# Kernel tuning notes

Hardware: AMD Instinct MI355X
Metric: run time of the kernel (lower is better)

The kernel has to match this reference:

```python
import jax, jax.numpy as jnp
import numpy as np

N_WIN = 7    # n_win hardcoded in AR_Attention
TOPK = 4     # topk routing windows
HEADS = 8    # num_heads


def setup_inputs() -> dict:
    key = jax.random.key(0)
    ks = jax.random.split(key, 6)
    B, H, W, C = 4, 56, 56, 256
    s = 0.02
    x = jax.random.normal(ks[0], (B, H, W, C), jnp.float32)
    Wqkv = jax.random.normal(ks[1], (C, 3 * C), jnp.float32) * s  # Linear(dim, 3*dim) (qk_dim=dim)
    bqkv = jnp.zeros((3 * C,), jnp.float32)
    Wo = jax.random.normal(ks[2], (C, C), jnp.float32) * s        # output projection Linear(dim, dim)
    bo = jnp.zeros((C,), jnp.float32)
    lepe_w = jax.random.normal(ks[3], (5, 5, 1, C), jnp.float32) * s  # 5x5 depthwise conv (side_dwconv=5)
    lepe_b = jnp.zeros((C,), jnp.float32)
    return {"x": x, "Wqkv": Wqkv, "bqkv": bqkv, "Wo": Wo, "bo": bo,
            "lepe_w": lepe_w, "lepe_b": lepe_b}


def reference(x, Wqkv, bqkv, Wo, bo, lepe_w, lepe_b):
    B, H, W, C = x.shape
    nw = N_WIN
    h, w = H // nw, W // nw           # region size (8x8)
    p2 = nw * nw                      # number of regions (49)
    hd = C // HEADS                   # head dim
    scale = float(C) ** -0.5          # qk_scale = qk_dim ** -0.5 (qk_dim = dim)

    # region partition: [B,H,W,C] -> [B,p2,h,w,C]
    xr = x.reshape(B, nw, h, nw, w, C).transpose(0, 1, 3, 2, 4, 5).reshape(B, p2, h, w, C)

    qkv = xr @ Wqkv + bqkv            # [B,p2,h,w,3C]
    q, kv = qkv[..., :C], qkv[..., C:]

    q_pix = q.reshape(B, p2, h * w, C)
    kv_pix = kv.reshape(B, p2, h * w, 2 * C)   # kv_downsample_mode='identity'

    # region-level queries/keys via per-window mean pooling
    q_win = q.mean((2, 3))                     # [B,p2,C]
    k_win = kv[..., :C].mean((2, 3))           # [B,p2,C]

    # LEPE: 5x5 depthwise conv on v over the full image grid
    v_img = kv[..., C:].reshape(B, nw, nw, h, w, C).transpose(0, 1, 3, 2, 4, 5).reshape(B, H, W, C)
    lepe = jax.lax.conv_general_dilated(
        v_img, lepe_w, (1, 1), 'SAME',
        dimension_numbers=('NHWC', 'HWIO', 'NHWC'),
        feature_group_count=C) + lepe_b

    # top-k window routing (param_routing=False, hard routing, mul_weight='none')
    r_logit = jnp.einsum('bpc,bqc->bpq', q_win * scale, k_win)  # [B,p2,p2]
    _, r_idx = jax.lax.top_k(r_logit, TOPK)                     # [B,p2,TOPK]

    # gather selected kv windows: [B,p2,TOPK,h*w,2C]
    kv_sel = jax.vmap(lambda kvp, i: kvp[i])(kv_pix, r_idx)

    k_sel = kv_sel[..., :C].reshape(B, p2, TOPK * h * w, HEADS, hd)
    v_sel = kv_sel[..., C:].reshape(B, p2, TOPK * h * w, HEADS, hd)
    qh = q_pix.reshape(B, p2, h * w, HEADS, hd)

    attn = jnp.einsum('bpqnd,bpknd->bpnqk', qh * scale, k_sel)  # [B,p2,heads,hw,TOPK*hw]
    attn = jax.nn.softmax(attn, axis=-1)
    out = jnp.einsum('bpnqk,bpknd->bpqnd', attn, v_sel).reshape(B, p2, h, w, C)

    # windows back to image grid
    out = out.reshape(B, nw, nw, h, w, C).transpose(0, 1, 3, 2, 4, 5).reshape(B, H, W, C)
    out = out + lepe
    return out @ Wo + bo
```

## Files before the change

kernel.cpp:

```cpp
#include <hip/hip_runtime.h>
#include <hip/hip_bf16.h>

#define NPIX 12544

typedef short bf16x8 __attribute__((ext_vector_type(8)));
typedef short bf16x4 __attribute__((ext_vector_type(4)));
typedef float f32x4  __attribute__((ext_vector_type(4)));

__device__ __forceinline__ float bf2f(unsigned short u) {
    unsigned int x = ((unsigned int)u) << 16;
    float f; __builtin_memcpy(&f, &x, sizeof(f)); return f;
}
__device__ __forceinline__ unsigned short f2bf(float f) {
    __hip_bfloat16 h = __float2bfloat16(f);
    unsigned short u; __builtin_memcpy(&u, &h, 2); return u;
}
__device__ __forceinline__ void load_lds16(const unsigned short* g, unsigned short* l) {
    __builtin_amdgcn_global_load_lds(
        (const __attribute__((address_space(1))) unsigned int*)g,
        (__attribute__((address_space(3))) unsigned int*)l,
        16, 0, 0);
}
__device__ __forceinline__ unsigned ldsoff(const void* p) {
    return (unsigned)(unsigned long long)(const __attribute__((address_space(3))) char*)p;
}
template<int OFF>
__device__ __forceinline__ bf16x4 tr16(unsigned addr) {
    bf16x4 d;
    asm volatile("ds_read_b64_tr_b16 %0, %1 offset:%c2"
                 : "=v"(d) : "v"(addr), "i"(OFF));
    return d;
}

__global__ __launch_bounds__(256) void k_prep(
    const float* __restrict__ X, unsigned short* __restrict__ Xb,
    float* __restrict__ xmean,
    const float* __restrict__ Wqkv, const float* __restrict__ Wo,
    unsigned short* __restrict__ Wtq, unsigned short* __restrict__ Wto)
{
    __shared__ __align__(16) unsigned char sm[64 * 65 * 4];
    const int t = threadIdx.x;
    const int blk = blockIdx.x;
    if (blk < 392) {
        float* part = (float*)sm;
        const int w = blk >> 1, hc = blk & 1;
        const int b = w / 49, p = w % 49;
        const int wi = p / 7, wj = p % 7;
        const int ch0 = hc * 128;
        const int ps = t >> 5, cg = t & 31;
        float4 s = {0.f, 0.f, 0.f, 0.f};
        #pragma unroll
        for (int i = 0; i < 8; i++) {
            int pp = ps * 8 + i;
            int y = wi * 8 + (pp >> 3), x = wj * 8 + (pp & 7);
            int idx = (((b * 56) + y) * 56 + x) * 256 + ch0 + cg * 4;
            float4 v = *reinterpret_cast<const float4*>(X + idx);
            s.x += v.x; s.y += v.y; s.z += v.z; s.w += v.w;
            ushort4 o = { f2bf(v.x), f2bf(v.y), f2bf(v.z), f2bf(v.w) };
            *reinterpret_cast<ushort4*>(Xb + idx) = o;
        }
        *reinterpret_cast<float4*>(part + t * 4) = *reinterpret_cast<float4*>(&s);
        __syncthreads();
        if (t < 32) {
            float4 m = {0.f, 0.f, 0.f, 0.f};
            #pragma unroll
            for (int ps2 = 0; ps2 < 8; ps2++) {
                float4 v = *reinterpret_cast<float4*>(part + (ps2 * 32 + t) * 4);
                m.x += v.x; m.y += v.y; m.z += v.z; m.w += v.w;
            }
            m.x *= (1.f / 64.f); m.y *= (1.f / 64.f);
            m.z *= (1.f / 64.f); m.w *= (1.f / 64.f);
            *reinterpret_cast<float4*>(xmean + w * 256 + ch0 + t * 4) = m;
        }
    } else {
        float* tile = (float*)sm;
        int tb = blk - 392;
        const float* Wsrc; unsigned short* Wdst; int N, kt, nt;
        if (tb < 48) { Wsrc = Wqkv; Wdst = Wtq; N = 768; kt = tb / 12; nt = tb % 12; }
        else { tb -= 48; Wsrc = Wo; Wdst = Wto; N = 256; kt = tb / 4; nt = tb % 4; }
        const int k0 = kt * 64, n0 = nt * 64;
        const int r0 = t >> 6, c = t & 63;
        #pragma unroll
        for (int i = 0; i < 16; i++) {
            int r = i * 4 + r0;
            tile[r * 65 + c] = Wsrc[(size_t)(k0 + r) * N + n0 + c];
        }
        __syncthreads();
        #pragma unroll
        for (int i = 0; i < 16; i++) {
            int n = i * 4 + r0;
            Wdst[(size_t)(n0 + n) * 256 + k0 + c] = f2bf(tile[c * 65 + n]);
        }
    }
}

__global__ __launch_bounds__(256) void k_main1(
    const unsigned short* __restrict__ A,
    const unsigned short* __restrict__ Bt,
    const float* __restrict__ bias,
    unsigned short* __restrict__ O,
    const float* __restrict__ xmean,
    const float* __restrict__ Wqkv,
    float* __restrict__ qwin, float* __restrict__ kwin)
{
    __shared__ __align__(16) unsigned char sm1[32768];
    const int t = threadIdx.x;
    const int blk = blockIdx.x;
    if (blk < 588) {
        unsigned short* As = (unsigned short*)sm1;
        unsigned short* Bs = (unsigned short*)(sm1 + 16384);
        const int m0 = (blk % 98) * 128, n0 = (blk / 98) * 128;
        const int wave = t >> 6, lane = t & 63, quad = lane >> 4, lo = lane & 15;
        const int wm = wave & 1, wn = wave >> 1;
        const int sr = wave * 16 + (lane >> 2);
        const int sc = lane & 3;
        f32x4 acc[4][4];
        #pragma unroll
        for (int i = 0; i < 4; i++)
            #pragma unroll
            for (int j = 0; j < 4; j++) acc[i][j] = (f32x4){0.f, 0.f, 0.f, 0.f};

        auto stage = [&](int it) {
            int kt = it * 32;
            unsigned short* Ad = As + (it & 1) * 4096;
            unsigned short* Bd = Bs + (it & 1) * 4096;
            #pragma unroll
            for (int j = 0; j < 2; j++) {
                int row = j * 64 + sr;
                int e = sc ^ ((row >> 1) & 3);
                load_lds16(A  + (size_t)(m0 + row) * 256 + kt + e * 8, &Ad[row * 32 + sc * 8]);
                load_lds16(Bt + (size_t)(n0 + row) * 256 + kt + e * 8, &Bd[row * 32 + sc * 8]);
            }
        };
        stage(0);
        for (int it = 0; it < 8; ++it) {
            if (it < 7) {
                stage(it + 1);
                asm volatile("s_waitcnt vmcnt(4)" ::: "memory");
            } else {
                asm volatile("s_waitcnt vmcnt(0)" ::: "memory");
            }
            __builtin_amdgcn_s_barrier();
            const unsigned short* Ac = As + (it & 1) * 4096;
            const unsigned short* Bc = Bs + (it & 1) * 4096;
            bf16x8 af[4], bfr[4];
            #pragma unroll
            for (int mt = 0; mt < 4; mt++) {
                int row = wm * 64 + mt * 16 + lo;
                int c = quad ^ ((row >> 1) & 3);
                af[mt] = *reinterpret_cast<const bf16x8*>(&Ac[row * 32 + c * 8]);
            }
            #pragma unroll
            for (int nt = 0; nt < 4; nt++) {
                int col = wn * 64 + nt * 16 + lo;
                int c = quad ^ ((col >> 1) & 3);
                bfr[nt] = *reinterpret_cast<const bf16x8*>(&Bc[col * 32 + c * 8]);
            }
            #pragma unroll
            for (int mt = 0; mt < 4; mt++)
                #pragma unroll
                for (int nt = 0; nt < 4; nt++)
                    acc[mt][nt] = __builtin_amdgcn_mfma_f32_16x16x32_bf16(
                        af[mt], bfr[nt], acc[mt][nt], 0, 0, 0);
            __builtin_amdgcn_s_barrier();
        }
        float bv[4];
        #pragma unroll
        for (int nt = 0; nt < 4; nt++) bv[nt] = bias[n0 + wn * 64 + nt * 16 + lo];
        #pragma unroll
        for (int mt = 0; mt < 4; mt++)
            #pragma unroll
            for (int nt = 0; nt < 4; nt++) {
                int n = n0 + wn * 64 + nt * 16 + lo;
                #pragma unroll
                for (int r = 0; r < 4; r++) {
                    int m = m0 + wm * 64 + mt * 16 + quad * 4 + r;
                    O[m * 768 + n] = f2bf(acc[mt][nt][r] + bv[nt]);
                }
            }
    } else {
        float* xs = (float*)sm1;
        const int u = blk - 588;
        const int bp = u % 196;
        const int half = u / 196;
        const int c = t;
        xs[c] = xmean[bp * 256 + c];
        __syncthreads();
        const int col = half * 256 + c;
        float a = 0.f;
        for (int k = 0; k < 256; k++) a += xs[k] * Wqkv[k * 768 + col];
        float* outp = half ? kwin : qwin;
        outp[bp * 256 + c] = a + bias[col];
    }
}

__global__ __launch_bounds__(256) void k_main2(
    const float* __restrict__ qwin, const float* __restrict__ kwin,
    int* __restrict__ ridx,
    const unsigned short* __restrict__ QKV,
    const float* __restrict__ lw, const float* __restrict__ lb,
    unsigned short* __restrict__ Olepe)
{
    __shared__ __align__(16) unsigned char sm2[25600];
    const int t = threadIdx.x;
    const int blk = blockIdx.x;
    if (blk < 196) {
        float* part = (float*)sm2;
        float* lg   = (float*)(sm2 + 49 * 4 * 4);
        const int b = blk / 49, p = blk % 49;
        if (t < 196) {
            int d = t >> 2, pr = t & 3;
            const float* qp = &qwin[(b * 49 + p) * 256];
            const float* kp = &kwin[(b * 49 + d) * 256];
            float a = 0.f;
            for (int ch = pr * 64; ch < pr * 64 + 64; ch++) a += qp[ch] * kp[ch];
            part[d * 4 + pr] = a;
        }
        __syncthreads();
        if (t < 49) lg[t] = part[t * 4 + 0] + part[t * 4 + 1] + part[t * 4 + 2] + part[t * 4 + 3];
        __syncthreads();
        if (t == 0) {
            unsigned long long used = 0ull;
            for (int sel = 0; sel < 4; sel++) {
                float best = -1e30f; int bi = 0;
                for (int qq = 0; qq < 49; qq++)
                    if (!((used >> qq) & 1ull) && lg[qq] > best) { best = lg[qq]; bi = qq; }
                used |= (1ull << bi);
                ridx[blk * 4 + sel] = bi;
            }
        }
    } else {
        float* lws = (float*)sm2;
        #pragma unroll
        for (int i = 0; i < 25; i++) lws[i * 256 + t] = lw[i * 256 + t];

        const int pl = t & 7;
        const int cg = t >> 3;
        const int c0 = cg * 8;
        const int gid = (blk - 196) * 8 + pl;
        const int b = gid / 3136, rem = gid % 3136;
        const int y = rem / 56, x = rem % 56;
        __syncthreads();

        float acc[8];
        {
            float4 b0 = *reinterpret_cast<const float4*>(lb + c0);
            float4 b1 = *reinterpret_cast<const float4*>(lb + c0 + 4);
            acc[0] = b0.x; acc[1] = b0.y; acc[2] = b0.z; acc[3] = b0.w;
            acc[4] = b1.x; acc[5] = b1.y; acc[6] = b1.z; acc[7] = b1.w;
        }
        #pragma unroll
        for (int ky = 0; ky < 5; ky++) {
            int yy = y + ky - 2;
            if (yy < 0 || yy >= 56) continue;
            #pragma unroll
            for (int kx = 0; kx < 5; kx++) {
                int xx = x + kx - 2;
                if (xx < 0 || xx >= 56) continue;
                bf16x8 v = *reinterpret_cast<const bf16x8*>(
                    QKV + (((b * 56) + yy) * 56 + xx) * 768 + 512 + c0);
                const float* wrow = &lws[(ky * 5 + kx) * 256 + c0];
                float4 w0 = *reinterpret_cast<const float4*>(wrow);
                float4 w1 = *reinterpret_cast<const float4*>(wrow + 4);
                acc[0] += bf2f((unsigned short)v[0]) * w0.x;
                acc[1] += bf2f((unsigned short)v[1]) * w0.y;
                acc[2] += bf2f((unsigned short)v[2]) * w0.z;
                acc[3] += bf2f((unsigned short)v[3]) * w0.w;
                acc[4] += bf2f((unsigned short)v[4]) * w1.x;
                acc[5] += bf2f((unsigned short)v[5]) * w1.y;
                acc[6] += bf2f((unsigned short)v[6]) * w1.z;
                acc[7] += bf2f((unsigned short)v[7]) * w1.w;
            }
        }
        bf16x8 o;
        #pragma unroll
        for (int j = 0; j < 8; j++) o[j] = (short)f2bf(acc[j]);
        *reinterpret_cast<bf16x8*>(Olepe + (size_t)gid * 256 + c0) = o;
    }
}

__global__ __launch_bounds__(256) void k_attn(
    const unsigned short* __restrict__ QKV,
    const int* __restrict__ ridx,
    const unsigned short* __restrict__ Olepe,
    unsigned short* __restrict__ Osum)
{
    __shared__ __align__(16) unsigned char smem[36864];
    unsigned short* Vs  = (unsigned short*)smem;
    unsigned short* Ks  = (unsigned short*)(smem + 16384);
    unsigned short* PST = (unsigned short*)(smem + 32768);

    const int p = blockIdx.x, head = blockIdx.y, b = blockIdx.z;
    const int t = threadIdx.x;
    const int wi = p / 7, wj = p % 7;
    const int wave = t >> 6, lane = t & 63, quad = lane >> 4, lo = lane & 15;
    const int pix4 = t >> 2, c4 = t & 3;

    const int q  = wave * 16 + lo;
    const int qy = wi * 8 + (q >> 3), qx = wj * 8 + (q & 7);

    bf16x8 af = *reinterpret_cast<const bf16x8*>(
        QKV + (size_t)(((b * 56) + qy) * 56 + qx) * 768 + head * 32 + quad * 8);

    {
        const int4 rs = *reinterpret_cast<const int4*>(&ridx[(b * 49 + p) * 4]);
        const int sels[4] = { rs.x, rs.y, rs.z, rs.w };
        #pragma unroll
        for (int pass = 0; pass < 4; pass++) {
            int sel = sels[pass];
            int si = sel / 7, sj = sel % 7;
            int y = si * 8 + (pix4 >> 3), x = sj * 8 + (pix4 & 7);
            const unsigned short* base = QKV + (((b * 56) + y) * 56 + x) * 768 + 256 + head * 32;
            bf16x8 kv = *reinterpret_cast<const bf16x8*>(base + c4 * 8);
            bf16x8 vv = *reinterpret_cast<const bf16x8*>(base + 256 + c4 * 8);
            int krow = pass * 64 + pix4;
            *reinterpret_cast<bf16x8*>(&Ks[krow * 32 + c4 * 8]) = kv;
            *reinterpret_cast<bf16x8*>(
                &Vs[(krow >> 2) * 128 + (c4 >> 1) * 64 + (krow & 3) * 16 + (c4 & 1) * 8]) = vv;
        }
    }
    __syncthreads();

    const f32x4 z = (f32x4){0.f, 0.f, 0.f, 0.f};

    float M[4] = {-1e30f, -1e30f, -1e30f, -1e30f};
    #pragma unroll 4
    for (int nt = 0; nt < 16; nt++) {
        bf16x8 bfr = *reinterpret_cast<const bf16x8*>(&Ks[(nt * 16 + lo) * 32 + quad * 8]);
        f32x4 s = __builtin_amdgcn_mfma_f32_16x16x32_bf16(af, bfr, z, 0, 0, 0);
        #pragma unroll
        for (int r = 0; r < 4; r++) M[r] = fmaxf(M[r], s[r] * 0.0625f);
    }
    #pragma unroll
    for (int d = 1; d < 16; d <<= 1)
        #pragma unroll
        for (int r = 0; r < 4; r++) M[r] = fmaxf(M[r], __shfl_xor(M[r], d));

    unsigned short* myP = PST + wave * 512;
    const unsigned pbase = ldsoff(myP) + quad * 256 + lo * 8;
    const unsigned vbase = ldsoff(Vs)  + quad * 512 + lo * 8;
    float l[4] = {0.f, 0.f, 0.f, 0.f};
    f32x4 o0 = z, o1 = z;
    for (int c = 0; c < 8; c++) {
        bf16x8 k0 = *reinterpret_cast<const bf16x8*>(&Ks[((2 * c) * 16 + lo) * 32 + quad * 8]);
        bf16x8 k1 = *reinterpret_cast<const bf16x8*>(&Ks[((2 * c + 1) * 16 + lo) * 32 + quad * 8]);
        f32x4 s0 = __builtin_amdgcn_mfma_f32_16x16x32_bf16(af, k0, z, 0, 0, 0);
        f32x4 s1 = __builtin_amdgcn_mfma_f32_16x16x32_bf16(af, k1, z, 0, 0, 0);
        float e0[4], e1[4];
        #pragma unroll
        for (int r = 0; r < 4; r++) {
            e0[r] = __expf(s0[r] * 0.0625f - M[r]);
            e1[r] = __expf(s1[r] * 0.0625f - M[r]);
            l[r] += e0[r] + e1[r];
        }
        ushort4 p0 = { f2bf(e0[0]), f2bf(e0[1]), f2bf(e0[2]), f2bf(e0[3]) };
        ushort4 p1 = { f2bf(e1[0]), f2bf(e1[1]), f2bf(e1[2]), f2bf(e1[3]) };
        *reinterpret_cast<ushort4*>(&myP[lo * 16 + quad * 4]) = p0;
        *reinterpret_cast<ushort4*>(&myP[(16 + lo) * 16 + quad * 4]) = p1;
        asm volatile("s_waitcnt lgkmcnt(0)" ::: "memory");
        __builtin_amdgcn_sched_barrier(0);

        const unsigned vb = vbase + c * 2048;
        bf16x4 ra0  = tr16<0>(pbase);
        bf16x4 ra1  = tr16<128>(pbase);
        bf16x4 rw00 = tr16<0>(vb);
        bf16x4 rw01 = tr16<256>(vb);
        bf16x4 rw10 = tr16<128>(vb);
        bf16x4 rw11 = tr16<384>(vb);
        asm volatile("s_waitcnt lgkmcnt(0)" ::: "memory");
        __builtin_amdgcn_sched_barrier(0);
        bf16x8 pa, vb0, vb1;
        #pragma unroll
        for (int j = 0; j < 4; j++) {
            pa[j]  = ra0[j];  pa[4 + j]  = ra1[j];
            vb0[j] = rw00[j]; vb0[4 + j] = rw01[j];
            vb1[j] = rw10[j]; vb1[4 + j] = rw11[j];
        }
        o0 = __builtin_amdgcn_mfma_f32_16x16x32_bf16(pa, vb0, o0, 0, 0, 0);
        o1 = __builtin_amdgcn_mfma_f32_16x16x32_bf16(pa, vb1, o1, 0, 0, 0);
    }
    #pragma unroll
    for (int d = 1; d < 16; d <<= 1)
        #pragma unroll
        for (int r = 0; r < 4; r++) l[r] += __shfl_xor(l[r], d);

    {
        float i0 = 1.f / l[0], i1 = 1.f / l[1], i2 = 1.f / l[2], i3 = 1.f / l[3];
        ushort4 p0 = { f2bf(o0[0] * i0), f2bf(o0[1] * i1),
                       f2bf(o0[2] * i2), f2bf(o0[3] * i3) };
        ushort4 p1 = { f2bf(o1[0] * i0), f2bf(o1[1] * i1),
                       f2bf(o1[2] * i2), f2bf(o1[3] * i3) };
        *reinterpret_cast<ushort4*>(&myP[lo * 16 + quad * 4]) = p0;
        *reinterpret_cast<ushort4*>(&myP[(16 + lo) * 16 + quad * 4]) = p1;
    }
    const unsigned oaddr = ldsoff(myP) + quad * 256 + lo * 8;
    asm volatile("s_waitcnt lgkmcnt(0)" ::: "memory");
    __builtin_amdgcn_sched_barrier(0);
    bf16x4 e0 = tr16<0>(oaddr);
    bf16x4 e1 = tr16<128>(oaddr);
    asm volatile("s_waitcnt lgkmcnt(0)" ::: "memory");
    __builtin_amdgcn_sched_barrier(0);
    {
        size_t gbase = (size_t)(((b * 56) + qy) * 56 + qx) * 256 + head * 32 + quad * 8;
        bf16x8 lp = *reinterpret_cast<const bf16x8*>(Olepe + gbase);
        bf16x8 oo;
        #pragma unroll
        for (int j = 0; j < 4; j++) {
            oo[j]     = (short)f2bf(bf2f((unsigned short)e0[j]) + bf2f((unsigned short)lp[j]));
            oo[4 + j] = (short)f2bf(bf2f((unsigned short)e1[j]) + bf2f((unsigned short)lp[4 + j]));
        }
        *reinterpret_cast<bf16x8*>(Osum + gbase) = oo;
    }
}

__global__ __launch_bounds__(256) void k_proj(
    const unsigned short* __restrict__ A,
    const unsigned short* __restrict__ Bt,
    const float* __restrict__ bias,
    float* __restrict__ O)
{
    __shared__ __align__(16) unsigned short As[2 * 128 * 32];
    __shared__ __align__(16) unsigned short Bs[2 * 64 * 32];
    const int t = threadIdx.x;
    const int m0 = blockIdx.x * 128, n0 = blockIdx.y * 64;
    const int wave = t >> 6, lane = t & 63, quad = lane >> 4, lo = lane & 15;
    const int sr = wave * 16 + (lane >> 2);
    const int sc = lane & 3;
    f32x4 acc[2][4];
    #pragma unroll
    for (int i = 0; i < 2; i++)
        #pragma unroll
        for (int j = 0; j < 4; j++) acc[i][j] = (f32x4){0.f, 0.f, 0.f, 0.f};

    auto stage = [&](int it) {
        int kt = it * 32;
        unsigned short* Ad = As + (it & 1) * 4096;
        unsigned short* Bd = Bs + (it & 1) * 2048;
        #pragma unroll
        for (int j = 0; j < 2; j++) {
            int row = j * 64 + sr;
            int e = sc ^ ((row >> 1) & 3);
            load_lds16(A + (size_t)(m0 + row) * 256 + kt + e * 8, &Ad[row * 32 + sc * 8]);
        }
        {
            int e = sc ^ ((sr >> 1) & 3);
            load_lds16(Bt + (size_t)(n0 + sr) * 256 + kt + e * 8, &Bd[sr * 32 + sc * 8]);
        }
    };
    stage(0);
    for (int it = 0; it < 8; ++it) {
        if (it < 7) {
            stage(it + 1);
            asm volatile("s_waitcnt vmcnt(3)" ::: "memory");
        } else {
            asm volatile("s_waitcnt vmcnt(0)" ::: "memory");
        }
        __builtin_amdgcn_s_barrier();
        const unsigned short* Ac = As + (it & 1) * 4096;
        const unsigned short* Bc = Bs + (it & 1) * 2048;
        bf16x8 af[2], bfr[4];
        #pragma unroll
        for (int mt = 0; mt < 2; mt++) {
            int row = wave * 32 + mt * 16 + lo;
            int c = quad ^ ((row >> 1) & 3);
            af[mt] = *reinterpret_cast<const bf16x8*>(&Ac[row * 32 + c * 8]);
        }
        #pragma unroll
        for (int nt = 0; nt < 4; nt++) {
            int col = nt * 16 + lo;
            int c = quad ^ ((col >> 1) & 3);
            bfr[nt] = *reinterpret_cast<const bf16x8*>(&Bc[col * 32 + c * 8]);
        }
        #pragma unroll
        for (int mt = 0; mt < 2; mt++)
            #pragma unroll
            for (int nt = 0; nt < 4; nt++)
                acc[mt][nt] = __builtin_amdgcn_mfma_f32_16x16x32_bf16(
                    af[mt], bfr[nt], acc[mt][nt], 0, 0, 0);
        __builtin_amdgcn_s_barrier();
    }
    float bv[4];
    #pragma unroll
    for (int nt = 0; nt < 4; nt++) bv[nt] = bias[n0 + nt * 16 + lo];
    #pragma unroll
    for (int mt = 0; mt < 2; mt++)
        #pragma unroll
        for (int nt = 0; nt < 4; nt++) {
            int n = n0 + nt * 16 + lo;
            #pragma unroll
            for (int r = 0; r < 4; r++) {
                int m = m0 + wave * 32 + mt * 16 + quad * 4 + r;
                O[m * 256 + n] = acc[mt][nt][r] + bv[nt];
            }
        }
}

extern "C" void kernel_launch(void* const* d_in, const int* in_sizes, int n_in,
                              void* d_out, int out_size, void* d_ws, size_t ws_size,
                              hipStream_t stream)
{
    const float* x    = (const float*)d_in[0];
    const float* Wqkv = (const float*)d_in[1];
    const float* bqkv = (const float*)d_in[2];
    const float* Wo   = (const float*)d_in[3];
    const float* bo   = (const float*)d_in[4];
    const float* lw   = (const float*)d_in[5];
    const float* lb   = (const float*)d_in[6];
    float* out = (float*)d_out;

    char* ws = (char*)d_ws;
    size_t off = 0;
    unsigned short* qkv   = (unsigned short*)(ws + off); off += (size_t)NPIX * 768 * 2;
    unsigned short* xb    = (unsigned short*)(ws + off); off += (size_t)NPIX * 256 * 2;
    unsigned short* Wtq   = (unsigned short*)(ws + off); off += 768 * 256 * 2;
    unsigned short* Wto   = (unsigned short*)(ws + off); off += 256 * 256 * 2;
    unsigned short* Osum  = (unsigned short*)(ws + off); off += (size_t)NPIX * 256 * 2;
    unsigned short* Olepe = (unsigned short*)(ws + off); off += (size_t)NPIX * 256 * 2;
    float* xmean = (float*)(ws + off); off += 196 * 256 * 4;
    float* qwin  = (float*)(ws + off); off += 196 * 256 * 4;
    float* kwin  = (float*)(ws + off); off += 196 * 256 * 4;
    int*   ridx  = (int*)(ws + off);   off += 196 * 4 * 4;

    k_prep <<<dim3(456),      256, 0, stream>>>(x, xb, xmean, Wqkv, Wo, Wtq, Wto);
    k_main1<<<dim3(980),      256, 0, stream>>>(xb, Wtq, bqkv, qkv, xmean, Wqkv, qwin, kwin);
    k_main2<<<dim3(1764),     256, 0, stream>>>(qwin, kwin, ridx, qkv, lw, lb, Olepe);
    k_attn <<<dim3(49, 8, 4), 256, 0, stream>>>(qkv, ridx, Olepe, Osum);
    k_proj <<<dim3(98, 4),    256, 0, stream>>>(Osum, Wto, bo, out);
}
```

Before: 151.7 us.

## Co-schedule LePE conv with attention and fold the LePE add into the projection load

```diff
diff --git a/kernel.cpp b/kernel.cpp
--- a/kernel.cpp
+++ b/kernel.cpp
@@ -194,50 +194,180 @@
     }
 }
 
-__global__ __launch_bounds__(256) void k_main2(
+__global__ __launch_bounds__(256) void k_route(
     const float* __restrict__ qwin, const float* __restrict__ kwin,
-    int* __restrict__ ridx,
+    int* __restrict__ ridx)
+{
+    __shared__ __align__(16) unsigned char sm2[1024];
+    const int t = threadIdx.x;
+    const int blk = blockIdx.x;
+    float* part = (float*)sm2;
+    float* lg   = (float*)(sm2 + 49 * 4 * 4);
+    const int b = blk / 49, p = blk % 49;
+    if (t < 196) {
+        int d = t >> 2, pr = t & 3;
+        const float* qp = &qwin[(b * 49 + p) * 256];
+        const float* kp = &kwin[(b * 49 + d) * 256];
+        float a = 0.f;
+        for (int ch = pr * 64; ch < pr * 64 + 64; ch++) a += qp[ch] * kp[ch];
+        part[d * 4 + pr] = a;
+    }
+    __syncthreads();
+    if (t < 49) lg[t] = part[t * 4 + 0] + part[t * 4 + 1] + part[t * 4 + 2] + part[t * 4 + 3];
+    __syncthreads();
+    if (t == 0) {
+        unsigned long long used = 0ull;
+        for (int sel = 0; sel < 4; sel++) {
+            float best = -1e30f; int bi = 0;
+            for (int qq = 0; qq < 49; qq++)
+                if (!((used >> qq) & 1ull) && lg[qq] > best) { best = lg[qq]; bi = qq; }
+            used |= (1ull << bi);
+            ridx[blk * 4 + sel] = bi;
+        }
+    }
+}
+
+__global__ __launch_bounds__(256) void k_attn(
     const unsigned short* __restrict__ QKV,
+    const int* __restrict__ ridx,
     const float* __restrict__ lw, const float* __restrict__ lb,
+    unsigned short* __restrict__ Osum,
     unsigned short* __restrict__ Olepe)
 {
-    __shared__ __align__(16) unsigned char sm2[25600];
+    __shared__ __align__(16) unsigned char smem[36864];
     const int t = threadIdx.x;
     const int blk = blockIdx.x;
-    if (blk < 196) {
-        float* part = (float*)sm2;
-        float* lg   = (float*)(sm2 + 49 * 4 * 4);
-        const int b = blk / 49, p = blk % 49;
-        if (t < 196) {
-            int d = t >> 2, pr = t & 3;
-            const float* qp = &qwin[(b * 49 + p) * 256];
-            const float* kp = &kwin[(b * 49 + d) * 256];
-            float a = 0.f;
-            for (int ch = pr * 64; ch < pr * 64 + 64; ch++) a += qp[ch] * kp[ch];
-            part[d * 4 + pr] = a;
+
+    if (blk < 1568) {
+        unsigned short* Vs  = (unsigned short*)smem;
+        unsigned short* Ks  = (unsigned short*)(smem + 16384);
+        unsigned short* PST = (unsigned short*)(smem + 32768);
+
+        const int p = blk % 49, head = (blk / 49) % 8, b = blk / 392;
+        const int wi = p / 7, wj = p % 7;
+        const int wave = t >> 6, lane = t & 63, quad = lane >> 4, lo = lane & 15;
+        const int pix4 = t >> 2, c4 = t & 3;
+
+        const int q  = wave * 16 + lo;
+        const int qy = wi * 8 + (q >> 3), qx = wj * 8 + (q & 7);
+
+        bf16x8 af = *reinterpret_cast<const bf16x8*>(
+            QKV + (size_t)(((b * 56) + qy) * 56 + qx) * 768 + head * 32 + quad * 8);
+
+        {
+            const int4 rs = *reinterpret_cast<const int4*>(&ridx[(b * 49 + p) * 4]);
+            const int sels[4] = { rs.x, rs.y, rs.z, rs.w };
+            #pragma unroll
+            for (int pass = 0; pass < 4; pass++) {
+                int sel = sels[pass];
+                int si = sel / 7, sj = sel % 7;
+                int y = si * 8 + (pix4 >> 3), x = sj * 8 + (pix4 & 7);
+                const unsigned short* base = QKV + (((b * 56) + y) * 56 + x) * 768 + 256 + head * 32;
+                bf16x8 kv = *reinterpret_cast<const bf16x8*>(base + c4 * 8);
+                bf16x8 vv = *reinterpret_cast<const bf16x8*>(base + 256 + c4 * 8);
+                int krow = pass * 64 + pix4;
+                *reinterpret_cast<bf16x8*>(&Ks[krow * 32 + c4 * 8]) = kv;
+                *reinterpret_cast<bf16x8*>(
+                    &Vs[(krow >> 2) * 128 + (c4 >> 1) * 64 + (krow & 3) * 16 + (c4 & 1) * 8]) = vv;
+            }
         }
         __syncthreads();
-        if (t < 49) lg[t] = part[t * 4 + 0] + part[t * 4 + 1] + part[t * 4 + 2] + part[t * 4 + 3];
-        __syncthreads();
-        if (t == 0) {
-            unsigned long long used = 0ull;
-            for (int sel = 0; sel < 4; sel++) {
-                float best = -1e30f; int bi = 0;
-                for (int qq = 0; qq < 49; qq++)
-                    if (!((used >> qq) & 1ull) && lg[qq] > best) { best = lg[qq]; bi = qq; }
-                used |= (1ull << bi);
-                ridx[blk * 4 + sel] = bi;
-            }
+
+        const f32x4 z = (f32x4){0.f, 0.f, 0.f, 0.f};
+
+        float M[4] = {-1e30f, -1e30f, -1e30f, -1e30f};
+        #pragma unroll 4
+        for (int nt = 0; nt < 16; nt++) {
+            bf16x8 bfr = *reinterpret_cast<const bf16x8*>(&Ks[(nt * 16 + lo) * 32 + quad * 8]);
+            f32x4 s = __builtin_amdgcn_mfma_f32_16x16x32_bf16(af, bfr, z, 0, 0, 0);
+            #pragma unroll
+            for (int r = 0; r < 4; r++) M[r] = fmaxf(M[r], s[r] * 0.0625f);
+        }
+        #pragma unroll
+        for (int d = 1; d < 16; d <<= 1)
+            #pragma unroll
+            for (int r = 0; r < 4; r++) M[r] = fmaxf(M[r], __shfl_xor(M[r], d));
+
+        unsigned short* myP = PST + wave * 512;
+        const unsigned pbase = ldsoff(myP) + quad * 256 + lo * 8;
+        const unsigned vbase = ldsoff(Vs)  + quad * 512 + lo * 8;
+        float l[4] = {0.f, 0.f, 0.f, 0.f};
+        f32x4 o0 = z, o1 = z;
+        for (int c = 0; c < 8; c++) {
+            bf16x8 k0 = *reinterpret_cast<const bf16x8*>(&Ks[((2 * c) * 16 + lo) * 32 + quad * 8]);
+            bf16x8 k1 = *reinterpret_cast<const bf16x8*>(&Ks[((2 * c + 1) * 16 + lo) * 32 + quad * 8]);
+            f32x4 s0 = __builtin_amdgcn_mfma_f32_16x16x32_bf16(af, k0, z, 0, 0, 0);
+            f32x4 s1 = __builtin_amdgcn_mfma_f32_16x16x32_bf16(af, k1, z, 0, 0, 0);
+            float e0[4], e1[4];
+            #pragma unroll
+            for (int r = 0; r < 4; r++) {
+                e0[r] = __expf(s0[r] * 0.0625f - M[r]);
+                e1[r] = __expf(s1[r] * 0.0625f - M[r]);
+                l[r] += e0[r] + e1[r];
+            }
+            ushort4 p0 = { f2bf(e0[0]), f2bf(e0[1]), f2bf(e0[2]), f2bf(e0[3]) };
+            ushort4 p1 = { f2bf(e1[0]), f2bf(e1[1]), f2bf(e1[2]), f2bf(e1[3]) };
+            *reinterpret_cast<ushort4*>(&myP[lo * 16 + quad * 4]) = p0;
+            *reinterpret_cast<ushort4*>(&myP[(16 + lo) * 16 + quad * 4]) = p1;
+            asm volatile("s_waitcnt lgkmcnt(0)" ::: "memory");
+            __builtin_amdgcn_sched_barrier(0);
+
+            const unsigned vb = vbase + c * 2048;
+            bf16x4 ra0  = tr16<0>(pbase);
+            bf16x4 ra1  = tr16<128>(pbase);
+            bf16x4 rw00 = tr16<0>(vb);
+            bf16x4 rw01 = tr16<256>(vb);
+            bf16x4 rw10 = tr16<128>(vb);
+            bf16x4 rw11 = tr16<384>(vb);
+            asm volatile("s_waitcnt lgkmcnt(0)" ::: "memory");
+            __builtin_amdgcn_sched_barrier(0);
+            bf16x8 pa, vb0, vb1;
+            #pragma unroll
+            for (int j = 0; j < 4; j++) {
+                pa[j]  = ra0[j];  pa[4 + j]  = ra1[j];
+                vb0[j] = rw00[j]; vb0[4 + j] = rw01[j];
+                vb1[j] = rw10[j]; vb1[4 + j] = rw11[j];
+            }
+            o0 = __builtin_amdgcn_mfma_f32_16x16x32_bf16(pa, vb0, o0, 0, 0, 0);
+            o1 = __builtin_amdgcn_mfma_f32_16x16x32_bf16(pa, vb1, o1, 0, 0, 0);
+        }
+        #pragma unroll
+        for (int d = 1; d < 16; d <<= 1)
+            #pragma unroll
+            for (int r = 0; r < 4; r++) l[r] += __shfl_xor(l[r], d);
+
+        {
+            float i0 = 1.f / l[0], i1 = 1.f / l[1], i2 = 1.f / l[2], i3 = 1.f / l[3];
+            ushort4 p0 = { f2bf(o0[0] * i0), f2bf(o0[1] * i1),
+                           f2bf(o0[2] * i2), f2bf(o0[3] * i3) };
+            ushort4 p1 = { f2bf(o1[0] * i0), f2bf(o1[1] * i1),
+                           f2bf(o1[2] * i2), f2bf(o1[3] * i3) };
+            *reinterpret_cast<ushort4*>(&myP[lo * 16 + quad * 4]) = p0;
+            *reinterpret_cast<ushort4*>(&myP[(16 + lo) * 16 + quad * 4]) = p1;
+        }
+        const unsigned oaddr = ldsoff(myP) + quad * 256 + lo * 8;
+        asm volatile("s_waitcnt lgkmcnt(0)" ::: "memory");
+        __builtin_amdgcn_sched_barrier(0);
+        bf16x4 e0 = tr16<0>(oaddr);
+        bf16x4 e1 = tr16<128>(oaddr);
+        asm volatile("s_waitcnt lgkmcnt(0)" ::: "memory");
+        __builtin_amdgcn_sched_barrier(0);
+        {
+            size_t gbase = (size_t)(((b * 56) + qy) * 56 + qx) * 256 + head * 32 + quad * 8;
+            bf16x8 oo;
+            #pragma unroll
+            for (int j = 0; j < 4; j++) { oo[j] = e0[j]; oo[4 + j] = e1[j]; }
+            *reinterpret_cast<bf16x8*>(Osum + gbase) = oo;
         }
     } else {
-        float* lws = (float*)sm2;
+        float* lws = (float*)smem;
         #pragma unroll
         for (int i = 0; i < 25; i++) lws[i * 256 + t] = lw[i * 256 + t];
 
         const int pl = t & 7;
         const int cg = t >> 3;
         const int c0 = cg * 8;
-        const int gid = (blk - 196) * 8 + pl;
+        const int gid = (blk - 1568) * 8 + pl;
         const int b = gid / 3136, rem = gid % 3136;
         const int y = rem / 56, x = rem % 56;
         __syncthreads();
@@ -279,142 +409,9 @@
     }
 }
 
-__global__ __launch_bounds__(256) void k_attn(
-    const unsigned short* __restrict__ QKV,
-    const int* __restrict__ ridx,
-    const unsigned short* __restrict__ Olepe,
-    unsigned short* __restrict__ Osum)
-{
-    __shared__ __align__(16) unsigned char smem[36864];
-    unsigned short* Vs  = (unsigned short*)smem;
-    unsigned short* Ks  = (unsigned short*)(smem + 16384);
-    unsigned short* PST = (unsigned short*)(smem + 32768);
-
-    const int p = blockIdx.x, head = blockIdx.y, b = blockIdx.z;
-    const int t = threadIdx.x;
-    const int wi = p / 7, wj = p % 7;
-    const int wave = t >> 6, lane = t & 63, quad = lane >> 4, lo = lane & 15;
-    const int pix4 = t >> 2, c4 = t & 3;
-
-    const int q  = wave * 16 + lo;
-    const int qy = wi * 8 + (q >> 3), qx = wj * 8 + (q & 7);
-
-    bf16x8 af = *reinterpret_cast<const bf16x8*>(
-        QKV + (size_t)(((b * 56) + qy) * 56 + qx) * 768 + head * 32 + quad * 8);
-
-    {
-        const int4 rs = *reinterpret_cast<const int4*>(&ridx[(b * 49 + p) * 4]);
-        const int sels[4] = { rs.x, rs.y, rs.z, rs.w };
-        #pragma unroll
-        for (int pass = 0; pass < 4; pass++) {
-            int sel = sels[pass];
-            int si = sel / 7, sj = sel % 7;
-            int y = si * 8 + (pix4 >> 3), x = sj * 8 + (pix4 & 7);
-            const unsigned short* base = QKV + (((b * 56) + y) * 56 + x) * 768 + 256 + head * 32;
-            bf16x8 kv = *reinterpret_cast<const bf16x8*>(base + c4 * 8);
-            bf16x8 vv = *reinterpret_cast<const bf16x8*>(base + 256 + c4 * 8);
-            int krow = pass * 64 + pix4;
-            *reinterpret_cast<bf16x8*>(&Ks[krow * 32 + c4 * 8]) = kv;
-            *reinterpret_cast<bf16x8*>(
-                &Vs[(krow >> 2) * 128 + (c4 >> 1) * 64 + (krow & 3) * 16 + (c4 & 1) * 8]) = vv;
-        }
-    }
-    __syncthreads();
-
-    const f32x4 z = (f32x4){0.f, 0.f, 0.f, 0.f};
-
-    float M[4] = {-1e30f, -1e30f, -1e30f, -1e30f};
-    #pragma unroll 4
-    for (int nt = 0; nt < 16; nt++) {
-        bf16x8 bfr = *reinterpret_cast<const bf16x8*>(&Ks[(nt * 16 + lo) * 32 + quad * 8]);
-        f32x4 s = __builtin_amdgcn_mfma_f32_16x16x32_bf16(af, bfr, z, 0, 0, 0);
-        #pragma unroll
-        for (int r = 0; r < 4; r++) M[r] = fmaxf(M[r], s[r] * 0.0625f);
-    }
-    #pragma unroll
-    for (int d = 1; d < 16; d <<= 1)
-        #pragma unroll
-        for (int r = 0; r < 4; r++) M[r] = fmaxf(M[r], __shfl_xor(M[r], d));
-
-    unsigned short* myP = PST + wave * 512;
-    const unsigned pbase = ldsoff(myP) + quad * 256 + lo * 8;
-    const unsigned vbase = ldsoff(Vs)  + quad * 512 + lo * 8;
-    float l[4] = {0.f, 0.f, 0.f, 0.f};
-    f32x4 o0 = z, o1 = z;
-    for (int c = 0; c < 8; c++) {
-        bf16x8 k0 = *reinterpret_cast<const bf16x8*>(&Ks[((2 * c) * 16 + lo) * 32 + quad * 8]);
-        bf16x8 k1 = *reinterpret_cast<const bf16x8*>(&Ks[((2 * c + 1) * 16 + lo) * 32 + quad * 8]);
-        f32x4 s0 = __builtin_amdgcn_mfma_f32_16x16x32_bf16(af, k0, z, 0, 0, 0);
-        f32x4 s1 = __builtin_amdgcn_mfma_f32_16x16x32_bf16(af, k1, z, 0, 0, 0);
-        float e0[4], e1[4];
-        #pragma unroll
-        for (int r = 0; r < 4; r++) {
-            e0[r] = __expf(s0[r] * 0.0625f - M[r]);
-            e1[r] = __expf(s1[r] * 0.0625f - M[r]);
-            l[r] += e0[r] + e1[r];
-        }
-        ushort4 p0 = { f2bf(e0[0]), f2bf(e0[1]), f2bf(e0[2]), f2bf(e0[3]) };
-        ushort4 p1 = { f2bf(e1[0]), f2bf(e1[1]), f2bf(e1[2]), f2bf(e1[3]) };
-        *reinterpret_cast<ushort4*>(&myP[lo * 16 + quad * 4]) = p0;
-        *reinterpret_cast<ushort4*>(&myP[(16 + lo) * 16 + quad * 4]) = p1;
-        asm volatile("s_waitcnt lgkmcnt(0)" ::: "memory");
-        __builtin_amdgcn_sched_barrier(0);
-
-        const unsigned vb = vbase + c * 2048;
-        bf16x4 ra0  = tr16<0>(pbase);
-        bf16x4 ra1  = tr16<128>(pbase);
-        bf16x4 rw00 = tr16<0>(vb);
-        bf16x4 rw01 = tr16<256>(vb);
-        bf16x4 rw10 = tr16<128>(vb);
-        bf16x4 rw11 = tr16<384>(vb);
-        asm volatile("s_waitcnt lgkmcnt(0)" ::: "memory");
-        __builtin_amdgcn_sched_barrier(0);
-        bf16x8 pa, vb0, vb1;
-        #pragma unroll
-        for (int j = 0; j < 4; j++) {
-            pa[j]  = ra0[j];  pa[4 + j]  = ra1[j];
-            vb0[j] = rw00[j]; vb0[4 + j] = rw01[j];
-            vb1[j] = rw10[j]; vb1[4 + j] = rw11[j];
-        }
-        o0 = __builtin_amdgcn_mfma_f32_16x16x32_bf16(pa, vb0, o0, 0, 0, 0);
-        o1 = __builtin_amdgcn_mfma_f32_16x16x32_bf16(pa, vb1, o1, 0, 0, 0);
-    }
-    #pragma unroll
-    for (int d = 1; d < 16; d <<= 1)
-        #pragma unroll
-        for (int r = 0; r < 4; r++) l[r] += __shfl_xor(l[r], d);
-
-    {
-        float i0 = 1.f / l[0], i1 = 1.f / l[1], i2 = 1.f / l[2], i3 = 1.f / l[3];
-        ushort4 p0 = { f2bf(o0[0] * i0), f2bf(o0[1] * i1),
-                       f2bf(o0[2] * i2), f2bf(o0[3] * i3) };
-        ushort4 p1 = { f2bf(o1[0] * i0), f2bf(o1[1] * i1),
-                       f2bf(o1[2] * i2), f2bf(o1[3] * i3) };
-        *reinterpret_cast<ushort4*>(&myP[lo * 16 + quad * 4]) = p0;
-        *reinterpret_cast<ushort4*>(&myP[(16 + lo) * 16 + quad * 4]) = p1;
-    }
-    const unsigned oaddr = ldsoff(myP) + quad * 256 + lo * 8;
-    asm volatile("s_waitcnt lgkmcnt(0)" ::: "memory");
-    __builtin_amdgcn_sched_barrier(0);
-    bf16x4 e0 = tr16<0>(oaddr);
-    bf16x4 e1 = tr16<128>(oaddr);
-    asm volatile("s_waitcnt lgkmcnt(0)" ::: "memory");
-    __builtin_amdgcn_sched_barrier(0);
-    {
-        size_t gbase = (size_t)(((b * 56) + qy) * 56 + qx) * 256 + head * 32 + quad * 8;
-        bf16x8 lp = *reinterpret_cast<const bf16x8*>(Olepe + gbase);
-        bf16x8 oo;
-        #pragma unroll
-        for (int j = 0; j < 4; j++) {
-            oo[j]     = (short)f2bf(bf2f((unsigned short)e0[j]) + bf2f((unsigned short)lp[j]));
-            oo[4 + j] = (short)f2bf(bf2f((unsigned short)e1[j]) + bf2f((unsigned short)lp[4 + j]));
-        }
-        *reinterpret_cast<bf16x8*>(Osum + gbase) = oo;
-    }
-}
-
 __global__ __launch_bounds__(256) void k_proj(
-    const unsigned short* __restrict__ A,
+    const unsigned short* __restrict__ S,
+    const unsigned short* __restrict__ L,
     const unsigned short* __restrict__ Bt,
     const float* __restrict__ bias,
     float* __restrict__ O)
@@ -426,35 +423,52 @@
     const int wave = t >> 6, lane = t & 63, quad = lane >> 4, lo = lane & 15;
     const int sr = wave * 16 + (lane >> 2);
     const int sc = lane & 3;
+    const int e  = sc ^ ((sr >> 1) & 3);
     f32x4 acc[2][4];
     #pragma unroll
     for (int i = 0; i < 2; i++)
         #pragma unroll
         for (int j = 0; j < 4; j++) acc[i][j] = (f32x4){0.f, 0.f, 0.f, 0.f};
 
-    auto stage = [&](int it) {
+    bf16x8 s0a, l0a, s1a, l1a;
+    bf16x8 s0b, l0b, s1b, l1b;
+
+    auto issueA = [&](int it, bf16x8& s0, bf16x8& l0, bf16x8& s1, bf16x8& l1) {
         int kt = it * 32;
+        size_t base0 = (size_t)(m0 + sr) * 256 + kt + sc * 8;
+        size_t base1 = (size_t)(m0 + 64 + sr) * 256 + kt + sc * 8;
+        s0 = *reinterpret_cast<const bf16x8*>(S + base0);
+        l0 = *reinterpret_cast<const bf16x8*>(L + base0);
+        s1 = *reinterpret_cast<const bf16x8*>(S + base1);
+        l1 = *reinterpret_cast<const bf16x8*>(L + base1);
+    };
+    auto issueB = [&](int it) {
+        int kt = it * 32;
+        unsigned short* Bd = Bs + (it & 1) * 2048;
+        load_lds16(Bt + (size_t)(n0 + sr) * 256 + kt + e * 8, &Bd[sr * 32 + sc * 8]);
+    };
+    auto writeA = [&](int it, bf16x8& s0, bf16x8& l0, bf16x8& s1, bf16x8& l1) {
         unsigned short* Ad = As + (it & 1) * 4096;
-        unsigned short* Bd = Bs + (it & 1) * 2048;
-        #pragma unroll
-        for (int j = 0; j < 2; j++) {
-            int row = j * 64 + sr;
-            int e = sc ^ ((row >> 1) & 3);
-            load_lds16(A + (size_t)(m0 + row) * 256 + kt + e * 8, &Ad[row * 32 + sc * 8]);
-        }
-        {
-            int e = sc ^ ((sr >> 1) & 3);
-            load_lds16(Bt + (size_t)(n0 + sr) * 256 + kt + e * 8, &Bd[sr * 32 + sc * 8]);
-        }
+        bf16x8 a0, a1;
+        #pragma unroll
+        for (int j = 0; j < 8; j++) {
+            a0[j] = (short)f2bf(bf2f((unsigned short)s0[j]) + bf2f((unsigned short)l0[j]));
+            a1[j] = (short)f2bf(bf2f((unsigned short)s1[j]) + bf2f((unsigned short)l1[j]));
+        }
+        *reinterpret_cast<bf16x8*>(&Ad[sr * 32 + e * 8]) = a0;
+        *reinterpret_cast<bf16x8*>(&Ad[(64 + sr) * 32 + e * 8]) = a1;
     };
-    stage(0);
+
+    issueA(0, s0a, l0a, s1a, l1a); issueB(0);
     for (int it = 0; it < 8; ++it) {
         if (it < 7) {
-            stage(it + 1);
-            asm volatile("s_waitcnt vmcnt(3)" ::: "memory");
+            issueA(it + 1, s0b, l0b, s1b, l1b); issueB(it + 1);
+            asm volatile("s_waitcnt vmcnt(5)" ::: "memory");
         } else {
             asm volatile("s_waitcnt vmcnt(0)" ::: "memory");
         }
+        writeA(it, s0a, l0a, s1a, l1a);
+        asm volatile("s_waitcnt lgkmcnt(0)" ::: "memory");
         __builtin_amdgcn_s_barrier();
         const unsigned short* Ac = As + (it & 1) * 4096;
         const unsigned short* Bc = Bs + (it & 1) * 2048;
@@ -478,6 +492,7 @@
                 acc[mt][nt] = __builtin_amdgcn_mfma_f32_16x16x32_bf16(
                     af[mt], bfr[nt], acc[mt][nt], 0, 0, 0);
         __builtin_amdgcn_s_barrier();
+        s0a = s0b; l0a = l0b; s1a = s1b; l1a = l1b;
     }
     float bv[4];
     #pragma unroll
@@ -523,7 +538,7 @@
 
     k_prep <<<dim3(456),      256, 0, stream>>>(x, xb, xmean, Wqkv, Wo, Wtq, Wto);
     k_main1<<<dim3(980),      256, 0, stream>>>(xb, Wtq, bqkv, qkv, xmean, Wqkv, qwin, kwin);
-    k_main2<<<dim3(1764),     256, 0, stream>>>(qwin, kwin, ridx, qkv, lw, lb, Olepe);
-    k_attn <<<dim3(49, 8, 4), 256, 0, stream>>>(qkv, ridx, Olepe, Osum);
-    k_proj <<<dim3(98, 4),    256, 0, stream>>>(Osum, Wto, bo, out);
-}
+    k_route<<<dim3(196),      256, 0, stream>>>(qwin, kwin, ridx);
+    k_attn <<<dim3(3136),     256, 0, stream>>>(qkv, ridx, lw, lb, Osum, Olepe);
+    k_proj <<<dim3(98, 4),    256, 0, stream>>>(Osum, Olepe, Wto, bo, out);
+}
```

Result: slower. 161.0 us (+6.1%).
